# Kernel optimization log

Measured on AMD Instinct MI355X. Metric: run time of the kernel, lower is better.

## Reference

```python
import jax, jax.numpy as jnp
import numpy as np

RC = 5.0  # cosine cutoff radius

def ssp(z):
    # shifted softplus, SchNet activation
    return jax.nn.softplus(z) - jnp.log(2.0).astype(z.dtype)

def setup_inputs():
    key = jax.random.key(0)
    ks = jax.random.split(key, 16)
    B, Na, Nn, G, F = 2, 2048, 48, 50, 128
    e = jax.random.normal(ks[0], (B, Na, 1), jnp.float32)
    x = jax.random.normal(ks[1], (B, Na, F), jnp.float32)
    t = jax.random.normal(ks[2], (B, Na, 1), jnp.float32)
    r_ij = jax.random.uniform(ks[3], (B, Na, Nn), jnp.float32) * 6.0  # some beyond cutoff
    neighbors = jax.random.randint(ks[4], (B, Na, Nn), 0, Na)
    pairwise_mask = jax.random.randint(ks[5], (B, Na, Nn), 0, 2).astype(jnp.int32)
    f_ij = jax.random.normal(ks[6], (B, Na, Nn, G), jnp.float32)
    def lin(k, fan_in, fan_out):
        return jax.random.normal(k, (fan_in, fan_out), jnp.float32) / np.sqrt(fan_in).astype(np.float32)
    Wf1 = lin(ks[7], G, F); bf1 = jnp.zeros((F,), jnp.float32)
    Wf2 = lin(ks[8], F, F); bf2 = jnp.zeros((F,), jnp.float32)
    Wq = lin(ks[9], F, F)
    Wk = lin(ks[10], F, F)
    Wv = lin(ks[11], F, F)
    Wo = lin(ks[12], F, F); bo = jnp.zeros((F,), jnp.float32)
    return dict(e=e, x=x, t=t, r_ij=r_ij, neighbors=neighbors, pairwise_mask=pairwise_mask,
                f_ij=f_ij, Wf1=Wf1, bf1=bf1, Wf2=Wf2, bf2=bf2, Wq=Wq, Wk=Wk, Wv=Wv, Wo=Wo, bo=bo)

def reference(e, x, t, r_ij, neighbors, pairwise_mask, f_ij,
              Wf1, bf1, Wf2, bf2, Wq, Wk, Wv, Wo, bo):
    B, Na, Nn = neighbors.shape
    F = x.shape[-1]
    # continuous filter from expanded distances: W = filter_network(2*f_ij - 1)
    W = 2.0 * f_ij - 1.0
    W = ssp(W @ Wf1 + bf1) @ Wf2 + bf2                # [B,Na,Nn,F]
    # cosine cutoff
    C = (0.5 * (jnp.cos(jnp.pi * r_ij / RC) + 1.0) * (r_ij < RC))[..., None]  # [B,Na,Nn,1]
    W = W * C
    # gather neighbor embeddings: y[b,i,n,:] = x[b, neighbors[b,i,n], :]
    idx = neighbors.reshape(B, Na * Nn)
    y = jnp.take_along_axis(x, idx[..., None], axis=1).reshape(B, Na, Nn, F)
    y_full = jnp.concatenate([x[:, :, None, :], y], axis=2)  # [B,Na,Nn+1,F] self + neighbors
    # cutoff-masked attention aggregation
    q = x @ Wq                                        # [B,Na,F]
    k = y_full @ Wk                                   # [B,Na,Nn+1,F]
    v = y_full @ Wv
    v = jnp.concatenate([v[:, :, :1, :], v[:, :, 1:, :] * W], axis=2)  # filter-modulated values
    scores = jnp.einsum('baf,banf->ban', q, k) / jnp.sqrt(jnp.float32(F))
    mask = jnp.concatenate([jnp.ones((B, Na, 1), bool), pairwise_mask.astype(bool)], axis=2)
    scores = jnp.where(mask, scores, jnp.float32(-1e9))
    attn = jax.nn.softmax(scores, axis=-1)
    m = jnp.einsum('ban,banf->baf', attn, v)
    m = ssp(m @ Wo + bo)                              # [B,Na,F]
    return (m, W)
```

## Files before the change

### kernel.cpp

```cpp
#include <hip/hip_runtime.h>

typedef unsigned int uint;
typedef unsigned short ushort;

#define B_  2
#define NA  2048
#define NN  48
#define G_  50
#define F_  128
#define NK  49
#define NROW (B_ * NA * NN)
#define NAT  (B_ * NA)

typedef short short8 __attribute__((ext_vector_type(8)));
typedef float floatx4 __attribute__((ext_vector_type(4)));

__device__ __forceinline__ float ssp(float z) {
  return fmaxf(z, 0.f) + __logf(1.f + __expf(-fabsf(z))) - 0.69314718055994531f;
}
__device__ __forceinline__ ushort f2bf(float x) {
  union { float f; uint u; } v; v.f = x;
  uint u = v.u;
  u += 0x7fffu + ((u >> 16) & 1u);
  return (ushort)(u >> 16);
}
__device__ __forceinline__ uint pk2bf(float x, float y) {
  return (uint)f2bf(x) | ((uint)f2bf(y) << 16);
}

extern "C" __global__ __launch_bounds__(256)
void prep_kernel(const float* __restrict__ Wf1, const float* __restrict__ Wf2,
                 const float* __restrict__ Wv, const float* __restrict__ Wo,
                 ushort* __restrict__ Wf1t, ushort* __restrict__ Wf2t,
                 ushort* __restrict__ Wvt, ushort* __restrict__ Wot)
{
  int gid = blockIdx.x * 256 + threadIdx.x;
  if (gid < 8192) {
    int n = gid >> 6, k = gid & 63;
    Wf1t[gid] = f2bf((k < G_) ? Wf1[(size_t)k * F_ + n] : 0.f);
  }
  for (int idx = gid; idx < 3 * 16384; idx += 24576) {
    int m = idx >> 14, e = idx & 16383;
    int n = e >> 7, k = e & 127;
    const float* src = (m == 0) ? Wf2 : (m == 1) ? Wv : Wo;
    ushort* dst = (m == 0) ? Wf2t : (m == 1) ? Wvt : Wot;
    dst[e] = f2bf(src[(size_t)k * F_ + n]);
  }
}

extern "C" __global__ __launch_bounds__(256, 4)
void qk_kernel(const float* __restrict__ x,
               const float* __restrict__ Wq, const float* __restrict__ Wk,
               float* __restrict__ Qo, float* __restrict__ Ko)
{
  __shared__ float xs[32 * 128];
  const int t = threadIdx.x;
  const int f = t & 127, h = t >> 7;
  const size_t Rb = (size_t)blockIdx.x * 32;
  const float* W = blockIdx.y ? Wk : Wq;
  float* O = blockIdx.y ? Ko : Qo;

  {
    const float4* src = (const float4*)(x + Rb * F_);
    float4* dst = (float4*)xs;
    #pragma unroll
    for (int k = 0; k < 4; ++k) dst[t + 256 * k] = src[t + 256 * k];
  }
  __syncthreads();

  float acc[16];
  #pragma unroll
  for (int j = 0; j < 16; ++j) acc[j] = 0.f;
  #pragma unroll
  for (int kc = 0; kc < 4; ++kc) {
    float wr[32];
    #pragma unroll
    for (int kk = 0; kk < 32; ++kk) wr[kk] = W[(size_t)(kc * 32 + kk) * F_ + f];
    #pragma unroll
    for (int j = 0; j < 16; ++j) {
      const float4* xr = (const float4*)&xs[(h * 16 + j) * 128 + kc * 32];
      #pragma unroll
      for (int qq = 0; qq < 8; ++qq) {
        float4 v = xr[qq];
        acc[j] += v.x * wr[qq * 4] + v.y * wr[qq * 4 + 1]
                + v.z * wr[qq * 4 + 2] + v.w * wr[qq * 4 + 3];
      }
    }
  }
  #pragma unroll
  for (int j = 0; j < 16; ++j)
    O[(Rb + h * 16 + j) * F_ + f] = acc[j];
}

extern "C" __global__ __launch_bounds__(256, 4)
void v_kernel(const float* __restrict__ x, const ushort* __restrict__ Wvt,
              float* __restrict__ Vo)
{
  __shared__ ushort xb[16 * 136];
  const int t = threadIdx.x;
  const int lane = t & 63, w = t >> 6;
  const int c16 = lane & 15, q = lane >> 4;
  const size_t Rb = (size_t)blockIdx.x * 16;

  {
    int row = t >> 4, col = (t & 15) * 8;
    float4 v0 = *(const float4*)(x + (Rb + row) * F_ + col);
    float4 v1 = *(const float4*)(x + (Rb + row) * F_ + col + 4);
    uint4 pk = { pk2bf(v0.x, v0.y), pk2bf(v0.z, v0.w),
                 pk2bf(v1.x, v1.y), pk2bf(v1.z, v1.w) };
    *(uint4*)((char*)xb + row * 272 + col * 2) = pk;
  }
  __syncthreads();

  short8 a[4];
  const char* ap = (const char*)xb + c16 * 272 + q * 16;
  #pragma unroll
  for (int s = 0; s < 4; ++s) a[s] = *(const short8*)(ap + s * 64);

  #pragma unroll
  for (int u = 0; u < 2; ++u) {
    int n = (w * 2 + u) * 16 + c16;
    const char* bb = (const char*)Wvt + n * 256 + q * 16;
    floatx4 acc = {0.f, 0.f, 0.f, 0.f};
    #pragma unroll
    for (int s = 0; s < 4; ++s) {
      short8 b = *(const short8*)(bb + s * 64);
      acc = __builtin_amdgcn_mfma_f32_16x16x32_bf16(a[s], b, acc, 0, 0, 0);
    }
    #pragma unroll
    for (int r = 0; r < 4; ++r)
      Vo[(Rb + q * 4 + r) * F_ + n] = acc[r];
  }
}

struct __align__(16) SmemF {
  ushort ft[64 * 72];
  ushort h1[64 * 136];
  float  C[64];
};

extern "C" __global__ __launch_bounds__(256, 4)
void filter_kernel(const float* __restrict__ fij, const float* __restrict__ r_ij,
                   const ushort* __restrict__ Wf1t, const float* __restrict__ bf1,
                   const ushort* __restrict__ Wf2t, const float* __restrict__ bf2p,
                   float* __restrict__ out_W)
{
  __shared__ SmemF sm;
  const int t = threadIdx.x;
  const int lane = t & 63, w = t >> 6;
  const int m0 = w * 16;
  const int c16 = lane & 15, q = lane >> 4;
  const size_t Rb = (size_t)blockIdx.x * 64;

  for (int idx = t; idx < 64 * 32; idx += 256) {
    int row = idx >> 5, kp = idx & 31;
    uint pk = 0;
    if (kp < 25) {
      float2 v = *(const float2*)(fij + (Rb + row) * G_ + 2 * kp);
      pk = pk2bf(2.f * v.x - 1.f, 2.f * v.y - 1.f);
    }
    ((uint*)sm.ft)[row * 36 + kp] = pk;
  }
  if (t < 64) {
    float r = r_ij[Rb + t];
    sm.C[t] = (r < 5.0f) ? 0.5f * (cosf(0.62831853071795864769f * r) + 1.0f) : 0.0f;
  }
  __syncthreads();

  {
    const char* ap = (const char*)sm.ft + (m0 + c16) * 144 + q * 16;
    short8 a0 = *(const short8*)(ap);
    short8 a1 = *(const short8*)(ap + 64);
    #pragma unroll
    for (int nt = 0; nt < 8; ++nt) {
      int n = nt * 16 + c16;
      const char* bb = (const char*)Wf1t + n * 128 + q * 16;
      short8 b0 = *(const short8*)(bb);
      short8 b1 = *(const short8*)(bb + 64);
      floatx4 acc = {0.f, 0.f, 0.f, 0.f};
      acc = __builtin_amdgcn_mfma_f32_16x16x32_bf16(a0, b0, acc, 0, 0, 0);
      acc = __builtin_amdgcn_mfma_f32_16x16x32_bf16(a1, b1, acc, 0, 0, 0);
      float bias = bf1[n];
      #pragma unroll
      for (int r = 0; r < 4; ++r) {
        int row = m0 + q * 4 + r;
        sm.h1[row * 136 + n] = f2bf(ssp(acc[r] + bias));
      }
    }
  }
  __syncthreads();

  {
    short8 a[4];
    const char* ap = (const char*)sm.h1 + (m0 + c16) * 272 + q * 16;
    #pragma unroll
    for (int s = 0; s < 4; ++s) a[s] = *(const short8*)(ap + s * 64);
    #pragma unroll 2
    for (int nt = 0; nt < 8; ++nt) {
      int n = nt * 16 + c16;
      const char* bb = (const char*)Wf2t + n * 256 + q * 16;
      floatx4 acc = {0.f, 0.f, 0.f, 0.f};
      #pragma unroll
      for (int s = 0; s < 4; ++s) {
        short8 b = *(const short8*)(bb + s * 64);
        acc = __builtin_amdgcn_mfma_f32_16x16x32_bf16(a[s], b, acc, 0, 0, 0);
      }
      float bias = bf2p[n];
      #pragma unroll
      for (int r = 0; r < 4; ++r) {
        int row = m0 + q * 4 + r;
        out_W[(Rb + row) * F_ + n] = (acc[r] + bias) * sm.C[row];
      }
    }
  }
}

extern "C" __global__ __launch_bounds__(256, 4)
void attn_kernel(const float* __restrict__ Q, const float* __restrict__ K,
                 const float* __restrict__ V, const float* __restrict__ Wg,
                 const int* __restrict__ nbr, const int* __restrict__ pmask,
                 float* __restrict__ m_pre)
{
  const int t = threadIdx.x;
  const int lane = t & 63, w = t >> 6;
  const int a = blockIdx.x * 4 + w;
  const int b = a >> 11, i = a & 2047;
  const size_t base_nn = (size_t)a * NN;

  int nbrv = (lane < NN) ? nbr[base_nn + lane] : 0;
  int pmv  = (lane < NN) ? pmask[base_nn + lane] : 1;

  float2 q2 = *(const float2*)(Q + (size_t)a * F_ + lane * 2);

  float s_lane = -1e30f;
  #pragma unroll
  for (int n = 0; n < NK; ++n) {
    int src = (n == 0) ? i : __shfl(nbrv, (n > 0) ? n - 1 : 0);
    float2 k2 = *(const float2*)(K + ((size_t)b * NA + src) * F_ + lane * 2);
    float p = q2.x * k2.x + q2.y * k2.y;
    #pragma unroll
    for (int o = 32; o; o >>= 1) p += __shfl_xor(p, o);
    p *= 0.08838834764831845f;
    if (n > 0 && __shfl(pmv, n - 1) == 0) p = -1e9f;
    if (lane == n) s_lane = p;
  }

  float mx = s_lane;
  #pragma unroll
  for (int o = 32; o; o >>= 1) mx = fmaxf(mx, __shfl_xor(mx, o));
  float ev = (lane < NK) ? __expf(s_lane - mx) : 0.f;
  float sum = ev;
  #pragma unroll
  for (int o = 32; o; o >>= 1) sum += __shfl_xor(sum, o);
  float attn_l = ev / sum;

  float2 acc = {0.f, 0.f};
  #pragma unroll 8
  for (int n = 0; n < NK; ++n) {
    float an = __shfl(attn_l, n);
    int src = (n == 0) ? i : __shfl(nbrv, (n > 0) ? n - 1 : 0);
    float2 v2 = *(const float2*)(V + ((size_t)b * NA + src) * F_ + lane * 2);
    float2 w2 = {1.f, 1.f};
    if (n > 0) w2 = *(const float2*)(Wg + (base_nn + n - 1) * F_ + lane * 2);
    acc.x += an * w2.x * v2.x;
    acc.y += an * w2.y * v2.y;
  }
  *(float2*)(m_pre + (size_t)a * F_ + lane * 2) = acc;
}

extern "C" __global__ __launch_bounds__(256, 4)
void out_kernel(const float* __restrict__ m_pre, const ushort* __restrict__ Wot,
                const float* __restrict__ bo, float* __restrict__ out_m)
{
  __shared__ ushort xb[16 * 136];
  const int t = threadIdx.x;
  const int lane = t & 63, w = t >> 6;
  const int c16 = lane & 15, q = lane >> 4;
  const size_t Rb = (size_t)blockIdx.x * 16;

  {
    int row = t >> 4, col = (t & 15) * 8;
    float4 v0 = *(const float4*)(m_pre + (Rb + row) * F_ + col);
    float4 v1 = *(const float4*)(m_pre + (Rb + row) * F_ + col + 4);
    uint4 pk = { pk2bf(v0.x, v0.y), pk2bf(v0.z, v0.w),
                 pk2bf(v1.x, v1.y), pk2bf(v1.z, v1.w) };
    *(uint4*)((char*)xb + row * 272 + col * 2) = pk;
  }
  __syncthreads();

  short8 a[4];
  const char* ap = (const char*)xb + c16 * 272 + q * 16;
  #pragma unroll
  for (int s = 0; s < 4; ++s) a[s] = *(const short8*)(ap + s * 64);

  #pragma unroll
  for (int u = 0; u < 2; ++u) {
    int n = (w * 2 + u) * 16 + c16;
    const char* bb = (const char*)Wot + n * 256 + q * 16;
    floatx4 acc = {0.f, 0.f, 0.f, 0.f};
    #pragma unroll
    for (int s = 0; s < 4; ++s) {
      short8 b = *(const short8*)(bb + s * 64);
      acc = __builtin_amdgcn_mfma_f32_16x16x32_bf16(a[s], b, acc, 0, 0, 0);
    }
    float bias = bo[n];
    #pragma unroll
    for (int r = 0; r < 4; ++r)
      out_m[(Rb + q * 4 + r) * F_ + n] = ssp(acc[r] + bias);
  }
}

extern "C" void kernel_launch(void* const* d_in, const int* in_sizes, int n_in,
                              void* d_out, int out_size, void* d_ws, size_t ws_size,
                              hipStream_t stream) {
  const float* x   = (const float*)d_in[1];
  const float* r   = (const float*)d_in[3];
  const int*  nbr  = (const int*)d_in[4];
  const int*  pmk  = (const int*)d_in[5];
  const float* fij = (const float*)d_in[6];
  const float* Wf1 = (const float*)d_in[7];
  const float* bf1 = (const float*)d_in[8];
  const float* Wf2 = (const float*)d_in[9];
  const float* bf2p= (const float*)d_in[10];
  const float* Wq  = (const float*)d_in[11];
  const float* Wk  = (const float*)d_in[12];
  const float* Wv  = (const float*)d_in[13];
  const float* Wo  = (const float*)d_in[14];
  const float* bo  = (const float*)d_in[15];
  float* out_m = (float*)d_out;
  float* out_W = out_m + (size_t)NAT * F_;

  float* Qs = (float*)d_ws;
  float* Ks = Qs + (size_t)NAT * F_;
  float* Vs = Ks + (size_t)NAT * F_;
  float* Ms = Vs + (size_t)NAT * F_;
  ushort* Wf1t = (ushort*)(Ms + (size_t)NAT * F_);
  ushort* Wf2t = Wf1t + 128 * 64;
  ushort* Wvt  = Wf2t + 128 * 128;
  ushort* Wot  = Wvt  + 128 * 128;

  hipLaunchKernelGGL(prep_kernel, dim3(96), dim3(256), 0, stream,
                     Wf1, Wf2, Wv, Wo, Wf1t, Wf2t, Wvt, Wot);
  hipLaunchKernelGGL(qk_kernel, dim3(NAT / 32, 2), dim3(256), 0, stream,
                     x, Wq, Wk, Qs, Ks);
  hipLaunchKernelGGL(v_kernel, dim3(NAT / 16), dim3(256), 0, stream,
                     x, Wvt, Vs);
  hipLaunchKernelGGL(filter_kernel, dim3(NROW / 64), dim3(256), 0, stream,
                     fij, r, Wf1t, bf1, Wf2t, bf2p, out_W);
  hipLaunchKernelGGL(attn_kernel, dim3(NAT / 4), dim3(256), 0, stream,
                     Qs, Ks, Vs, out_W, nbr, pmk, Ms);
  hipLaunchKernelGGL(out_kernel, dim3(NAT / 16), dim3(256), 0, stream,
                     Ms, Wot, bo, out_m);
}
```

Baseline: 284.3 us.

## Double filter-kernel row tile to reuse weight fragments across two M-tiles

Each filter-network block now handles 128 rows instead of 64. Each wave computes two 16-row M-tiles, so Wf1 and Wf2 fragments loaded into registers are reused twice, which halves weight loads per row. The feature tile and hidden-activation buffers now share LDS through a union to limit shared-memory growth. The cost is more live registers per thread, with some risk of spills or lower occupancy, and half as many blocks in the grid.

```diff
diff --git a/kernel.cpp b/kernel.cpp
--- a/kernel.cpp
+++ b/kernel.cpp
@@ -133,10 +133,12 @@
   }
 }
 
-struct __align__(16) SmemF {
-  ushort ft[64 * 72];
-  ushort h1[64 * 136];
-  float  C[64];
+struct __align__(16) SmemF2 {
+  union {
+    ushort ft[128 * 72];
+    ushort h1[128 * 136];
+  } u;
+  float C[128];
 };
 
 extern "C" __global__ __launch_bounds__(256, 4)
@@ -145,71 +147,97 @@
                    const ushort* __restrict__ Wf2t, const float* __restrict__ bf2p,
                    float* __restrict__ out_W)
 {
-  __shared__ SmemF sm;
+  __shared__ SmemF2 sm;
   const int t = threadIdx.x;
   const int lane = t & 63, w = t >> 6;
-  const int m0 = w * 16;
   const int c16 = lane & 15, q = lane >> 4;
-  const size_t Rb = (size_t)blockIdx.x * 64;
-
-  for (int idx = t; idx < 64 * 32; idx += 256) {
+  const int m0 = w * 32;
+  const size_t Rb = (size_t)blockIdx.x * 128;
+
+  #pragma unroll
+  for (int it = 0; it < 16; ++it) {
+    int idx = t + it * 256;
     int row = idx >> 5, kp = idx & 31;
     uint pk = 0;
     if (kp < 25) {
       float2 v = *(const float2*)(fij + (Rb + row) * G_ + 2 * kp);
       pk = pk2bf(2.f * v.x - 1.f, 2.f * v.y - 1.f);
     }
-    ((uint*)sm.ft)[row * 36 + kp] = pk;
-  }
-  if (t < 64) {
+    ((uint*)sm.u.ft)[row * 36 + kp] = pk;
+  }
+  if (t < 128) {
     float r = r_ij[Rb + t];
     sm.C[t] = (r < 5.0f) ? 0.5f * (cosf(0.62831853071795864769f * r) + 1.0f) : 0.0f;
   }
   __syncthreads();
 
-  {
-    const char* ap = (const char*)sm.ft + (m0 + c16) * 144 + q * 16;
-    short8 a0 = *(const short8*)(ap);
-    short8 a1 = *(const short8*)(ap + 64);
-    #pragma unroll
-    for (int nt = 0; nt < 8; ++nt) {
-      int n = nt * 16 + c16;
-      const char* bb = (const char*)Wf1t + n * 128 + q * 16;
-      short8 b0 = *(const short8*)(bb);
-      short8 b1 = *(const short8*)(bb + 64);
+  short8 a1[2][2];
+  #pragma unroll
+  for (int mt = 0; mt < 2; ++mt) {
+    const char* ap = (const char*)sm.u.ft + (m0 + mt * 16 + c16) * 144 + q * 16;
+    a1[mt][0] = *(const short8*)(ap);
+    a1[mt][1] = *(const short8*)(ap + 64);
+  }
+  __syncthreads();
+
+  short8 b1[8][2];
+  #pragma unroll
+  for (int nt = 0; nt < 8; ++nt) {
+    const char* bb = (const char*)Wf1t + (nt * 16 + c16) * 128 + q * 16;
+    b1[nt][0] = *(const short8*)(bb);
+    b1[nt][1] = *(const short8*)(bb + 64);
+  }
+
+  #pragma unroll
+  for (int nt = 0; nt < 8; ++nt) {
+    int n = nt * 16 + c16;
+    float bias = bf1[n];
+    #pragma unroll
+    for (int mt = 0; mt < 2; ++mt) {
       floatx4 acc = {0.f, 0.f, 0.f, 0.f};
-      acc = __builtin_amdgcn_mfma_f32_16x16x32_bf16(a0, b0, acc, 0, 0, 0);
-      acc = __builtin_amdgcn_mfma_f32_16x16x32_bf16(a1, b1, acc, 0, 0, 0);
-      float bias = bf1[n];
+      acc = __builtin_amdgcn_mfma_f32_16x16x32_bf16(a1[mt][0], b1[nt][0], acc, 0, 0, 0);
+      acc = __builtin_amdgcn_mfma_f32_16x16x32_bf16(a1[mt][1], b1[nt][1], acc, 0, 0, 0);
       #pragma unroll
       for (int r = 0; r < 4; ++r) {
-        int row = m0 + q * 4 + r;
-        sm.h1[row * 136 + n] = f2bf(ssp(acc[r] + bias));
+        int row = m0 + mt * 16 + q * 4 + r;
+        sm.u.h1[row * 136 + n] = f2bf(ssp(acc[r] + bias));
       }
     }
   }
-  __syncthreads();
-
-  {
-    short8 a[4];
-    const char* ap = (const char*)sm.h1 + (m0 + c16) * 272 + q * 16;
-    #pragma unroll
-    for (int s = 0; s < 4; ++s) a[s] = *(const short8*)(ap + s * 64);
-    #pragma unroll 2
-    for (int nt = 0; nt < 8; ++nt) {
-      int n = nt * 16 + c16;
+
+  short8 a2[2][4];
+  #pragma unroll
+  for (int mt = 0; mt < 2; ++mt) {
+    const char* ap = (const char*)sm.u.h1 + (m0 + mt * 16 + c16) * 272 + q * 16;
+    #pragma unroll
+    for (int s = 0; s < 4; ++s) a2[mt][s] = *(const short8*)(ap + s * 64);
+  }
+
+  #pragma unroll
+  for (int g = 0; g < 2; ++g) {
+    short8 b2[4][4];
+    #pragma unroll
+    for (int j = 0; j < 4; ++j) {
+      int n = (g * 4 + j) * 16 + c16;
       const char* bb = (const char*)Wf2t + n * 256 + q * 16;
-      floatx4 acc = {0.f, 0.f, 0.f, 0.f};
       #pragma unroll
-      for (int s = 0; s < 4; ++s) {
-        short8 b = *(const short8*)(bb + s * 64);
-        acc = __builtin_amdgcn_mfma_f32_16x16x32_bf16(a[s], b, acc, 0, 0, 0);
-      }
+      for (int s = 0; s < 4; ++s) b2[j][s] = *(const short8*)(bb + s * 64);
+    }
+    #pragma unroll
+    for (int j = 0; j < 4; ++j) {
+      int n = (g * 4 + j) * 16 + c16;
       float bias = bf2p[n];
       #pragma unroll
-      for (int r = 0; r < 4; ++r) {
-        int row = m0 + q * 4 + r;
-        out_W[(Rb + row) * F_ + n] = (acc[r] + bias) * sm.C[row];
+      for (int mt = 0; mt < 2; ++mt) {
+        floatx4 acc = {0.f, 0.f, 0.f, 0.f};
+        #pragma unroll
+        for (int s = 0; s < 4; ++s)
+          acc = __builtin_amdgcn_mfma_f32_16x16x32_bf16(a2[mt][s], b2[j][s], acc, 0, 0, 0);
+        #pragma unroll
+        for (int r = 0; r < 4; ++r) {
+          int row = m0 + mt * 16 + q * 4 + r;
+          out_W[(Rb + row) * F_ + n] = (acc[r] + bias) * sm.C[row];
+        }
       }
     }
   }
@@ -345,7 +373,7 @@
                      x, Wq, Wk, Qs, Ks);
   hipLaunchKernelGGL(v_kernel, dim3(NAT / 16), dim3(256), 0, stream,
                      x, Wvt, Vs);
-  hipLaunchKernelGGL(filter_kernel, dim3(NROW / 64), dim3(256), 0, stream,
+  hipLaunchKernelGGL(filter_kernel, dim3(NROW / 128), dim3(256), 0, stream,
                      fij, r, Wf1t, bf1, Wf2t, bf2p, out_W);
   hipLaunchKernelGGL(attn_kernel, dim3(NAT / 4), dim3(256), 0, stream,
                      Qs, Ks, Vs, out_W, nbr, pmk, Ms);
```

After: 272.2 us. 4.2% less time.

## Alias filter LDS buffers, raise occupancy, transpose MFMA operands for vector stores

Applied to the files above, without the earlier changes.

The filter kernel now places the f_ij staging buffer and the hidden activation buffer in a union, which cuts LDS per block, and raises launch bounds to 8 blocks per CU. It also preloads Wf2 fragments in groups of four tiles to overlap the loads with MFMA work. The Wv and Wo projection kernels swap the MFMA A and B operands so each lane holds four consecutive columns, allowing one 16-byte vector store (and a vector bias load) instead of four scalar strided stores. The risks are register pressure under the tighter occupancy bound and the extra barrier needed before the aliased buffer is overwritten.

```diff
diff --git a/kernel.cpp b/kernel.cpp
--- a/kernel.cpp
+++ b/kernel.cpp
@@ -112,54 +112,56 @@
   }
   __syncthreads();
 
-  short8 a[4];
+  short8 bx[4];
   const char* ap = (const char*)xb + c16 * 272 + q * 16;
   #pragma unroll
-  for (int s = 0; s < 4; ++s) a[s] = *(const short8*)(ap + s * 64);
+  for (int s = 0; s < 4; ++s) bx[s] = *(const short8*)(ap + s * 64);
 
   #pragma unroll
   for (int u = 0; u < 2; ++u) {
-    int n = (w * 2 + u) * 16 + c16;
-    const char* bb = (const char*)Wvt + n * 256 + q * 16;
+    int ntile = w * 2 + u;
+    const char* bb = (const char*)Wvt + (ntile * 16 + c16) * 256 + q * 16;
     floatx4 acc = {0.f, 0.f, 0.f, 0.f};
     #pragma unroll
     for (int s = 0; s < 4; ++s) {
-      short8 b = *(const short8*)(bb + s * 64);
-      acc = __builtin_amdgcn_mfma_f32_16x16x32_bf16(a[s], b, acc, 0, 0, 0);
-    }
-    #pragma unroll
-    for (int r = 0; r < 4; ++r)
-      Vo[(Rb + q * 4 + r) * F_ + n] = acc[r];
-  }
-}
-
-struct __align__(16) SmemF {
-  ushort ft[64 * 72];
-  ushort h1[64 * 136];
-  float  C[64];
+      short8 wf = *(const short8*)(bb + s * 64);
+      acc = __builtin_amdgcn_mfma_f32_16x16x32_bf16(wf, bx[s], acc, 0, 0, 0);
+    }
+    *(floatx4*)(Vo + (Rb + c16) * F_ + ntile * 16 + q * 4) = acc;
+  }
+}
+
+struct __align__(16) SmemF3 {
+  union {
+    ushort ft[64 * 72];
+    ushort h1[64 * 136];
+  } u;
+  float C[64];
 };
 
-extern "C" __global__ __launch_bounds__(256, 4)
+extern "C" __global__ __launch_bounds__(256, 8)
 void filter_kernel(const float* __restrict__ fij, const float* __restrict__ r_ij,
                    const ushort* __restrict__ Wf1t, const float* __restrict__ bf1,
                    const ushort* __restrict__ Wf2t, const float* __restrict__ bf2p,
                    float* __restrict__ out_W)
 {
-  __shared__ SmemF sm;
+  __shared__ SmemF3 sm;
   const int t = threadIdx.x;
   const int lane = t & 63, w = t >> 6;
+  const int c16 = lane & 15, q = lane >> 4;
   const int m0 = w * 16;
-  const int c16 = lane & 15, q = lane >> 4;
   const size_t Rb = (size_t)blockIdx.x * 64;
 
-  for (int idx = t; idx < 64 * 32; idx += 256) {
+  #pragma unroll
+  for (int it = 0; it < 8; ++it) {
+    int idx = t + it * 256;
     int row = idx >> 5, kp = idx & 31;
     uint pk = 0;
     if (kp < 25) {
       float2 v = *(const float2*)(fij + (Rb + row) * G_ + 2 * kp);
       pk = pk2bf(2.f * v.x - 1.f, 2.f * v.y - 1.f);
     }
-    ((uint*)sm.ft)[row * 36 + kp] = pk;
+    ((uint*)sm.u.ft)[row * 36 + kp] = pk;
   }
   if (t < 64) {
     float r = r_ij[Rb + t];
@@ -167,45 +169,56 @@
   }
   __syncthreads();
 
-  {
-    const char* ap = (const char*)sm.ft + (m0 + c16) * 144 + q * 16;
-    short8 a0 = *(const short8*)(ap);
-    short8 a1 = *(const short8*)(ap + 64);
-    #pragma unroll
-    for (int nt = 0; nt < 8; ++nt) {
-      int n = nt * 16 + c16;
-      const char* bb = (const char*)Wf1t + n * 128 + q * 16;
-      short8 b0 = *(const short8*)(bb);
-      short8 b1 = *(const short8*)(bb + 64);
-      floatx4 acc = {0.f, 0.f, 0.f, 0.f};
-      acc = __builtin_amdgcn_mfma_f32_16x16x32_bf16(a0, b0, acc, 0, 0, 0);
-      acc = __builtin_amdgcn_mfma_f32_16x16x32_bf16(a1, b1, acc, 0, 0, 0);
-      float bias = bf1[n];
+  short8 a1[2];
+  {
+    const char* ap = (const char*)sm.u.ft + (m0 + c16) * 144 + q * 16;
+    a1[0] = *(const short8*)(ap);
+    a1[1] = *(const short8*)(ap + 64);
+  }
+  __syncthreads();
+
+  #pragma unroll
+  for (int nt = 0; nt < 8; ++nt) {
+    int n = nt * 16 + c16;
+    const char* bb = (const char*)Wf1t + n * 128 + q * 16;
+    short8 b0 = *(const short8*)(bb);
+    short8 b1v = *(const short8*)(bb + 64);
+    float bias = bf1[n];
+    floatx4 acc = {0.f, 0.f, 0.f, 0.f};
+    acc = __builtin_amdgcn_mfma_f32_16x16x32_bf16(a1[0], b0, acc, 0, 0, 0);
+    acc = __builtin_amdgcn_mfma_f32_16x16x32_bf16(a1[1], b1v, acc, 0, 0, 0);
+    #pragma unroll
+    for (int r = 0; r < 4; ++r) {
+      int row = m0 + q * 4 + r;
+      sm.u.h1[row * 136 + n] = f2bf(ssp(acc[r] + bias));
+    }
+  }
+
+  short8 a2[4];
+  {
+    const char* ap = (const char*)sm.u.h1 + (m0 + c16) * 272 + q * 16;
+    #pragma unroll
+    for (int s = 0; s < 4; ++s) a2[s] = *(const short8*)(ap + s * 64);
+  }
+
+  #pragma unroll
+  for (int g = 0; g < 2; ++g) {
+    short8 b2[4][4];
+    #pragma unroll
+    for (int j = 0; j < 4; ++j) {
+      int n = (g * 4 + j) * 16 + c16;
+      const char* bb = (const char*)Wf2t + n * 256 + q * 16;
       #pragma unroll
-      for (int r = 0; r < 4; ++r) {
-        int row = m0 + q * 4 + r;
-        sm.h1[row * 136 + n] = f2bf(ssp(acc[r] + bias));
-      }
-    }
-  }
-  __syncthreads();
-
-  {
-    short8 a[4];
-    const char* ap = (const char*)sm.h1 + (m0 + c16) * 272 + q * 16;
-    #pragma unroll
-    for (int s = 0; s < 4; ++s) a[s] = *(const short8*)(ap + s * 64);
-    #pragma unroll 2
-    for (int nt = 0; nt < 8; ++nt) {
-      int n = nt * 16 + c16;
-      const char* bb = (const char*)Wf2t + n * 256 + q * 16;
+      for (int s = 0; s < 4; ++s) b2[j][s] = *(const short8*)(bb + s * 64);
+    }
+    #pragma unroll
+    for (int j = 0; j < 4; ++j) {
+      int n = (g * 4 + j) * 16 + c16;
+      float bias = bf2p[n];
       floatx4 acc = {0.f, 0.f, 0.f, 0.f};
       #pragma unroll
-      for (int s = 0; s < 4; ++s) {
-        short8 b = *(const short8*)(bb + s * 64);
-        acc = __builtin_amdgcn_mfma_f32_16x16x32_bf16(a[s], b, acc, 0, 0, 0);
-      }
-      float bias = bf2p[n];
+      for (int s = 0; s < 4; ++s)
+        acc = __builtin_amdgcn_mfma_f32_16x16x32_bf16(a2[s], b2[j][s], acc, 0, 0, 0);
       #pragma unroll
       for (int r = 0; r < 4; ++r) {
         int row = m0 + q * 4 + r;
@@ -288,25 +301,29 @@
   }
   __syncthreads();
 
-  short8 a[4];
+  short8 bx[4];
   const char* ap = (const char*)xb + c16 * 272 + q * 16;
   #pragma unroll
-  for (int s = 0; s < 4; ++s) a[s] = *(const short8*)(ap + s * 64);
+  for (int s = 0; s < 4; ++s) bx[s] = *(const short8*)(ap + s * 64);
 
   #pragma unroll
   for (int u = 0; u < 2; ++u) {
-    int n = (w * 2 + u) * 16 + c16;
-    const char* bb = (const char*)Wot + n * 256 + q * 16;
+    int ntile = w * 2 + u;
+    const char* bb = (const char*)Wot + (ntile * 16 + c16) * 256 + q * 16;
     floatx4 acc = {0.f, 0.f, 0.f, 0.f};
     #pragma unroll
     for (int s = 0; s < 4; ++s) {
-      short8 b = *(const short8*)(bb + s * 64);
-      acc = __builtin_amdgcn_mfma_f32_16x16x32_bf16(a[s], b, acc, 0, 0, 0);
-    }
-    float bias = bo[n];
-    #pragma unroll
-    for (int r = 0; r < 4; ++r)
-      out_m[(Rb + q * 4 + r) * F_ + n] = ssp(acc[r] + bias);
+      short8 wf = *(const short8*)(bb + s * 64);
+      acc = __builtin_amdgcn_mfma_f32_16x16x32_bf16(wf, bx[s], acc, 0, 0, 0);
+    }
+    int n0 = ntile * 16 + q * 4;
+    float4 bv = *(const float4*)&bo[n0];
+    floatx4 outv;
+    outv[0] = ssp(acc[0] + bv.x);
+    outv[1] = ssp(acc[1] + bv.y);
+    outv[2] = ssp(acc[2] + bv.z);
+    outv[3] = ssp(acc[3] + bv.w);
+    *(floatx4*)(out_m + (Rb + c16) * F_ + n0) = outv;
   }
 }
 
```

New measurement: 299.2 us. 5.2% more time.
